# Kernel optimization log

Measured on AMD Instinct MI355X. Metric: run time of the kernel, lower is better.

## Reference

```python
import jax, jax.numpy as jnp
import numpy as np

N, DIM, HEADS, DH, WS = 32768, 1024, 8, 64, 256
INNER = HEADS * DH
MASK_VAL = -1e10  # ATTN_MASK_VALUE
EPS = 1e-5


def setup_inputs() -> dict:
    key = jax.random.key(0)
    k0, k1, k2 = jax.random.split(key, 3)
    x = jax.random.normal(k0, (N, DIM), jnp.float32)
    # rotary sin/cos with interleaved-pair layout matching rotate_every_two
    inv_freq = 1.0 / (10000.0 ** (jnp.arange(0, DH, 2, dtype=jnp.float32) / DH))
    freqs = jnp.arange(N, dtype=jnp.float32)[:, None] * inv_freq[None, :]  # [N, DH/2]
    sin = jnp.repeat(jnp.sin(freqs), 2, axis=-1)  # [N, DH]
    cos = jnp.repeat(jnp.cos(freqs), 2, axis=-1)  # [N, DH]
    gamma = jnp.ones((DIM,), jnp.float32)
    beta = jnp.zeros((DIM,), jnp.float32)
    w_qkv = jax.random.normal(k1, (DIM, 3 * INNER), jnp.float32) * 0.02
    w_out = jax.random.normal(k2, (INNER, DIM), jnp.float32) * 0.02
    b_out = jnp.zeros((DIM,), jnp.float32)
    return dict(x=x, sin=sin, cos=cos, gamma=gamma, beta=beta,
                w_qkv=w_qkv, w_out=w_out, b_out=b_out)


def _rotate_every_two(t):
    t1, t2 = t[..., 0::2], t[..., 1::2]
    return jnp.stack((-t2, t1), axis=-1).reshape(t.shape)


def _apply_rotary(t, sin, cos):
    # rot_dim == DH (full rotary), so no pass-through slice needed
    return t * cos + _rotate_every_two(t) * sin


def reference(x, sin, cos, gamma, beta, w_qkv, w_out, b_out):
    # LayerNorm (elementwise affine)
    mu = jnp.mean(x, axis=-1, keepdims=True)
    var = jnp.var(x, axis=-1, keepdims=True)
    x = (x - mu) * jax.lax.rsqrt(var + EPS) * gamma + beta
    # token shift: shift first half of channels by one token
    half = DIM // 2
    x_shift = jnp.pad(x[:, :half], ((1, 0), (0, 0)))[:-1]
    x = jnp.concatenate([x_shift, x[:, half:]], axis=-1)
    # qkv projection (no bias)
    qkv = x @ w_qkv  # [N, 3*INNER]
    q, k, v = jnp.split(qkv, 3, axis=-1)
    to_heads = lambda t: t.reshape(N, HEADS, DH).transpose(1, 0, 2)  # [H, N, DH]
    q, k, v = to_heads(q), to_heads(k), to_heads(v)
    # inline rotary on q, k AND v (as in source)
    q = _apply_rotary(q, sin, cos)
    k = _apply_rotary(k, sin, cos)
    v = _apply_rotary(v, sin, cos)
    # window split: [H, w, WS, DH]
    w = N // WS
    q, k, v = (t.reshape(HEADS, w, WS, DH) for t in (q, k, v))
    # look-back: each window attends to (previous window ++ current window)
    def lookback(t):
        t = jnp.pad(t, ((0, 0), (1, 0), (0, 0), (0, 0)))  # zero window at front
        return jnp.concatenate([t[:, :-1], t[:, 1:]], axis=2)  # [H, w, 2*WS, DH]
    k, v = lookback(k), lookback(v)
    sim = jnp.einsum('hwid,hwjd->hwij', q, k) * (DH ** -0.5)  # [H, w, WS, 2*WS]
    mask = jnp.tril(jnp.ones((WS, 2 * WS), dtype=bool), k=WS)  # j <= i + WS (causal)
    sim = jnp.where(mask, sim, MASK_VAL)
    attn = jax.nn.softmax(sim, axis=-1)
    out = jnp.einsum('hwij,hwjd->hwid', attn, v)  # [H, w, WS, DH]
    out = out.transpose(1, 2, 0, 3).reshape(N, INNER)  # '(w n) (h d)'
    return out @ w_out + b_out
```

## Files before the change

### kernel.cpp

```cpp
#include <hip/hip_runtime.h>

typedef __attribute__((ext_vector_type(4))) unsigned short us4;
typedef __attribute__((ext_vector_type(8))) unsigned short us8;
typedef __attribute__((ext_vector_type(8))) short s8;
typedef __attribute__((ext_vector_type(4))) float f32x4;
typedef __attribute__((ext_vector_type(16))) float f32x16;

#define NTOK 32768
#define DIM_ 1024
#define HEADS_ 8
#define DH_ 64
#define WS_ 256
#define NWIN_ 128
#define INNER_ 512

__device__ __forceinline__ float b2f(unsigned short u) {
  union { unsigned u; float f; } x; x.u = ((unsigned)u) << 16; return x.f;
}
__device__ __forceinline__ unsigned short f2b(float f) {
  union { float f; unsigned u; } x; x.f = f;
  unsigned r = x.u + 0x7FFFu + ((x.u >> 16) & 1u);
  return (unsigned short)(r >> 16);
}
__device__ __forceinline__ unsigned pk2(float a, float b) {
  return (unsigned)f2b(a) | ((unsigned)f2b(b) << 16);
}
__device__ __forceinline__ s8 mk_s8(unsigned w0, unsigned w1, unsigned w2, unsigned w3) {
  union { unsigned u[4]; s8 v; } x;
  x.u[0] = w0; x.u[1] = w1; x.u[2] = w2; x.u[3] = w3;
  return x.v;
}

__device__ __forceinline__ void gload_lds16(const unsigned short* g, void* l) {
  __builtin_amdgcn_global_load_lds((const __attribute__((address_space(1))) void*)g,
                                   (__attribute__((address_space(3))) void*)l, 16, 0, 0);
}

__global__ __launch_bounds__(256) void ln_shift(const float* __restrict__ x,
                                                const float* __restrict__ gamma,
                                                const float* __restrict__ beta,
                                                unsigned short* __restrict__ xs) {
  int row = blockIdx.x;
  int t = threadIdx.x;
  f32x4 v = ((const f32x4*)(x + (size_t)row * DIM_))[t];
  float sum = 0.f, ss = 0.f;
#pragma unroll
  for (int j = 0; j < 4; j++) { sum += v[j]; ss += v[j] * v[j]; }
#pragma unroll
  for (int off = 32; off >= 1; off >>= 1) {
    sum += __shfl_xor(sum, off);
    ss  += __shfl_xor(ss, off);
  }
  __shared__ float red[2][4];
  int wave = t >> 6, l = t & 63;
  if (l == 0) { red[0][wave] = sum; red[1][wave] = ss; }
  __syncthreads();
  sum = red[0][0] + red[0][1] + red[0][2] + red[0][3];
  ss  = red[1][0] + red[1][1] + red[1][2] + red[1][3];
  float mu = sum * (1.0f / DIM_);
  float var = ss * (1.0f / DIM_) - mu * mu;
  float rs = rsqrtf(var + 1e-5f);
  f32x4 g = ((const f32x4*)gamma)[t];
  f32x4 bb = ((const f32x4*)beta)[t];
  us4 o;
#pragma unroll
  for (int j = 0; j < 4; j++) o[j] = f2b((v[j] - mu) * rs * g[j] + bb[j]);
  int c0 = t * 4;
  if (c0 >= 512) {
    *(us4*)(xs + (size_t)row * DIM_ + c0) = o;
  } else {
    if (row + 1 < NTOK) *(us4*)(xs + (size_t)(row + 1) * DIM_ + c0) = o;
    if (row == 0) { us4 z = {0, 0, 0, 0}; *(us4*)(xs + c0) = z; }
  }
}

__global__ __launch_bounds__(256) void transpose_f32_bf16(const float* __restrict__ in,
                                                          unsigned short* __restrict__ out,
                                                          int R, int C) {
  __shared__ unsigned short tile[32][33];
  int bx = blockIdx.x * 32, by = blockIdx.y * 32;
  int tx = threadIdx.x, ty = threadIdx.y;
#pragma unroll
  for (int i = 0; i < 32; i += 8) tile[ty + i][tx] = f2b(in[(size_t)(by + ty + i) * C + bx + tx]);
  __syncthreads();
#pragma unroll
  for (int i = 0; i < 32; i += 8) out[(size_t)(bx + ty + i) * R + by + tx] = tile[tx][ty + i];
}

template <bool F32OUT>
__global__ __launch_bounds__(512, 2) void gemm_nt_pipe(const unsigned short* __restrict__ A,
                                                       const unsigned short* __restrict__ Bt,
                                                       void* __restrict__ Cv,
                                                       const float* __restrict__ bias,
                                                       int M, int N, int K) {
  __shared__ __align__(16) char lds[131072];
  int t = threadIdx.x;
  int l = t & 63, lg = l >> 4, ll = l & 15;
  int wave = t >> 6;
  int wm = wave >> 2, wn = wave & 3;

  int nbx = gridDim.x;
  int nwg = nbx * gridDim.y;
  int flat = blockIdx.y * nbx + blockIdx.x;
  int swz = (flat & 7) * (nwg >> 3) + (flat >> 3);
  int m0 = (swz / nbx) * 256, n0 = (swz % nbx) * 256;

  const f32x4 fz = {0.f, 0.f, 0.f, 0.f};
  f32x4 acc[8][4];
#pragma unroll
  for (int m = 0; m < 8; m++)
#pragma unroll
    for (int n = 0; n < 4; n++) acc[m][n] = fz;

  int srow = t >> 2;
  int sunit = (t & 3) ^ ((t >> 3) & 3);
  const unsigned short* gA = A + (size_t)(m0 + srow) * K + sunit * 8;
  const unsigned short* gB = Bt + (size_t)(n0 + srow) * K + sunit * 8;
  char* myA = lds + wave * 1024;
  char* myB = lds + 16384 + wave * 1024;

  int fsw = (ll >> 1) & 3;
  int nk = K >> 5;

#pragma unroll
  for (int s = 0; s < 3; s++) {
    gload_lds16(gA + s * 32, myA + s * 32768);
    gload_lds16(gA + s * 32 + (size_t)128 * K, myA + s * 32768 + 8192);
    gload_lds16(gB + s * 32, myB + s * 32768);
    gload_lds16(gB + s * 32 + (size_t)128 * K, myB + s * 32768 + 8192);
  }

  for (int kt = 0; kt < nk - 3; ++kt) {
    const char* sa = lds + (kt & 3) * 32768;
    const char* sb = sa + 16384;
    int pslot = ((kt + 3) & 3) * 32768;
    gload_lds16(gA + (kt + 3) * 32, myA + pslot);
    gload_lds16(gA + (kt + 3) * 32 + (size_t)128 * K, myA + pslot + 8192);
    asm volatile("s_waitcnt vmcnt(10)" ::: "memory");
    __builtin_amdgcn_s_barrier();
    __builtin_amdgcn_sched_barrier(0);
    s8 af[4], bf[4];
#pragma unroll
    for (int n = 0; n < 4; n++) {
      int r = wn * 64 + n * 16 + ll;
      bf[n] = *(const s8*)(sb + r * 64 + ((lg ^ fsw) << 4));
    }
#pragma unroll
    for (int m = 0; m < 4; m++) {
      int r = wm * 128 + m * 16 + ll;
      af[m] = *(const s8*)(sa + r * 64 + ((lg ^ fsw) << 4));
    }
    __builtin_amdgcn_s_setprio(1);
#pragma unroll
    for (int m = 0; m < 4; m++)
#pragma unroll
      for (int n = 0; n < 4; n++)
        acc[m][n] = __builtin_amdgcn_mfma_f32_16x16x32_bf16(af[m], bf[n], acc[m][n], 0, 0, 0);
    __builtin_amdgcn_s_setprio(0);
    gload_lds16(gB + (kt + 3) * 32, myB + pslot);
    gload_lds16(gB + (kt + 3) * 32 + (size_t)128 * K, myB + pslot + 8192);
    s8 af2[4];
#pragma unroll
    for (int m = 0; m < 4; m++) {
      int r = wm * 128 + 64 + m * 16 + ll;
      af2[m] = *(const s8*)(sa + r * 64 + ((lg ^ fsw) << 4));
    }
    __builtin_amdgcn_s_setprio(1);
#pragma unroll
    for (int m = 0; m < 4; m++)
#pragma unroll
      for (int n = 0; n < 4; n++)
        acc[m + 4][n] = __builtin_amdgcn_mfma_f32_16x16x32_bf16(af2[m], bf[n], acc[m + 4][n], 0, 0, 0);
    __builtin_amdgcn_s_setprio(0);
    __builtin_amdgcn_sched_barrier(0);
    __builtin_amdgcn_s_barrier();
  }

  asm volatile("s_waitcnt vmcnt(0)" ::: "memory");
  __builtin_amdgcn_s_barrier();
  __builtin_amdgcn_sched_barrier(0);
  for (int kt = nk - 3; kt < nk; ++kt) {
    const char* sa = lds + (kt & 3) * 32768;
    const char* sb = sa + 16384;
    s8 af[4], bf[4], af2[4];
#pragma unroll
    for (int n = 0; n < 4; n++) {
      int r = wn * 64 + n * 16 + ll;
      bf[n] = *(const s8*)(sb + r * 64 + ((lg ^ fsw) << 4));
    }
#pragma unroll
    for (int m = 0; m < 4; m++) {
      int r = wm * 128 + m * 16 + ll;
      af[m] = *(const s8*)(sa + r * 64 + ((lg ^ fsw) << 4));
    }
#pragma unroll
    for (int m = 0; m < 4; m++) {
      int r = wm * 128 + 64 + m * 16 + ll;
      af2[m] = *(const s8*)(sa + r * 64 + ((lg ^ fsw) << 4));
    }
#pragma unroll
    for (int m = 0; m < 4; m++)
#pragma unroll
      for (int n = 0; n < 4; n++)
        acc[m][n] = __builtin_amdgcn_mfma_f32_16x16x32_bf16(af[m], bf[n], acc[m][n], 0, 0, 0);
#pragma unroll
    for (int m = 0; m < 4; m++)
#pragma unroll
      for (int n = 0; n < 4; n++)
        acc[m + 4][n] = __builtin_amdgcn_mfma_f32_16x16x32_bf16(af2[m], bf[n], acc[m + 4][n], 0, 0, 0);
  }

#pragma unroll
  for (int n = 0; n < 4; n++) {
    int col = n0 + wn * 64 + n * 16 + ll;
    float bs = bias ? bias[col] : 0.0f;
#pragma unroll
    for (int m = 0; m < 8; m++) {
#pragma unroll
      for (int r = 0; r < 4; r++) {
        int row = m0 + wm * 128 + m * 16 + lg * 4 + r;
        if (F32OUT) ((float*)Cv)[(size_t)row * N + col] = acc[m][n][r] + bs;
        else ((unsigned short*)Cv)[(size_t)row * N + col] = f2b(acc[m][n][r] + bs);
      }
    }
  }
}

__global__ __launch_bounds__(256) void rotary_qk(const unsigned short* __restrict__ qkv,
                                                 const float* __restrict__ sn,
                                                 const float* __restrict__ cs,
                                                 unsigned short* __restrict__ qh,
                                                 unsigned short* __restrict__ kh) {
  int gid = blockIdx.x * 256 + threadIdx.x;
  int n = gid >> 7;
  int col = (gid & 127) * 8;
  int d = col & 63;
  us8 v = *(const us8*)(qkv + (size_t)n * 1536 + col);
  float se[8], ce[8];
  *(f32x4*)se = *(const f32x4*)(sn + (size_t)n * 64 + d);
  *(f32x4*)(se + 4) = *(const f32x4*)(sn + (size_t)n * 64 + d + 4);
  *(f32x4*)ce = *(const f32x4*)(cs + (size_t)n * 64 + d);
  *(f32x4*)(ce + 4) = *(const f32x4*)(cs + (size_t)n * 64 + d + 4);
  us8 o;
#pragma unroll
  for (int p = 0; p < 4; p++) {
    float v0 = b2f(v[2 * p]), v1 = b2f(v[2 * p + 1]);
    o[2 * p]     = f2b(v0 * ce[2 * p] - v1 * se[2 * p]);
    o[2 * p + 1] = f2b(v1 * ce[2 * p + 1] + v0 * se[2 * p + 1]);
  }
  int third = col >> 9;
  int cw = col & 511;
  int h = cw >> 6;
  unsigned short* dst = third ? kh : qh;
  *(us8*)(dst + ((size_t)h * NTOK + n) * 64 + (cw & 63)) = o;
}

__global__ __launch_bounds__(256) void rotary_vT(const unsigned short* __restrict__ qkv,
                                                 const float* __restrict__ sn,
                                                 const float* __restrict__ cs,
                                                 unsigned short* __restrict__ vt) {
  __shared__ unsigned short tile[64][72];
  int nt = blockIdx.x, h = blockIdx.y;
  int t = threadIdx.x;
  int i = t >> 2;
  int cc = (t & 3) * 16;
  int n = nt * 64 + i;
  const unsigned short* src = qkv + (size_t)n * 1536 + 1024 + h * 64 + cc;
  us8 v0 = *(const us8*)src;
  us8 v1 = *(const us8*)(src + 8);
  float se[16], ce[16];
#pragma unroll
  for (int q = 0; q < 4; q++) {
    *(f32x4*)(se + 4 * q) = *(const f32x4*)(sn + (size_t)n * 64 + cc + 4 * q);
    *(f32x4*)(ce + 4 * q) = *(const f32x4*)(cs + (size_t)n * 64 + cc + 4 * q);
  }
#pragma unroll
  for (int p = 0; p < 4; p++) {
    float a0 = b2f(v0[2 * p]), a1 = b2f(v0[2 * p + 1]);
    tile[i][cc + 2 * p]     = f2b(a0 * ce[2 * p] - a1 * se[2 * p]);
    tile[i][cc + 2 * p + 1] = f2b(a1 * ce[2 * p + 1] + a0 * se[2 * p + 1]);
    float b0 = b2f(v1[2 * p]), b1 = b2f(v1[2 * p + 1]);
    tile[i][cc + 8 + 2 * p]     = f2b(b0 * ce[8 + 2 * p] - b1 * se[8 + 2 * p]);
    tile[i][cc + 8 + 2 * p + 1] = f2b(b1 * ce[8 + 2 * p + 1] + b0 * se[8 + 2 * p + 1]);
  }
  __syncthreads();
  int dd = t >> 2;
  int nc = (t & 3) * 16;
  us8 r0, r1;
#pragma unroll
  for (int j = 0; j < 8; j++) { r0[j] = tile[nc + j][dd]; r1[j] = tile[nc + 8 + j][dd]; }
  unsigned short* dst = vt + ((size_t)h * 64 + dd) * NTOK + (size_t)nt * 64 + nc;
  *(us8*)dst = r0;
  *(us8*)(dst + 8) = r1;
}

__global__ __launch_bounds__(256, 4) void attn_kernel(const unsigned short* __restrict__ qh,
                                                      const unsigned short* __restrict__ kh,
                                                      const unsigned short* __restrict__ vt,
                                                      unsigned short* __restrict__ ao) {
  __shared__ char kbuf[2][8192];
  __shared__ char vbuf[8192];
  int half = blockIdx.x, w = blockIdx.y, h = blockIdx.z;
  int t = threadIdx.x;
  int wave = t >> 6, l = t & 63;
  int l31 = l & 31, hi = l >> 5;
  const unsigned short* qb = qh + (size_t)h * NTOK * 64;
  const unsigned short* kb = kh + (size_t)h * NTOK * 64;
  const unsigned short* vb = vt + (size_t)h * 64 * NTOK;

  int qw = half * 128 + wave * 32 + l31;
  int qn = w * 256 + qw;
  s8 qf[4];
#pragma unroll
  for (int dht = 0; dht < 4; dht++)
    qf[dht] = *(const s8*)(qb + (size_t)qn * 64 + dht * 16 + hi * 8);

  f32x16 o0 = {}, o1 = {};
  float dsum = (w == 0) ? 128.f : 0.f;
  int n0 = w * 256 - 256;
  int c0 = (w == 0) ? 4 : 0;

  int srow = wave * 16 + (l >> 3);
  int sunit = l & 7;

  {
    const unsigned short* g = kb + (size_t)(n0 + c0 * 64 + srow) * 64 + ((sunit ^ (srow & 7)) * 8);
    gload_lds16(g, kbuf[c0 & 1] + wave * 2048);
    gload_lds16(g + 8 * 64, kbuf[c0 & 1] + wave * 2048 + 1024);
  }
  __syncthreads();

  for (int c = c0; c < 8; ++c) {
    int cb = n0 + c * 64;
    {
      int d = srow;
      const unsigned short* g = vb + (size_t)d * NTOK + cb + ((sunit ^ (d & 7)) * 8);
      gload_lds16(g, vbuf + wave * 2048);
      gload_lds16(g + (size_t)8 * NTOK, vbuf + wave * 2048 + 1024);
    }
    if (c < 7) {
      const unsigned short* g = kb + (size_t)(cb + 64 + srow) * 64 + ((sunit ^ (srow & 7)) * 8);
      gload_lds16(g, kbuf[(c + 1) & 1] + wave * 2048);
      gload_lds16(g + 8 * 64, kbuf[(c + 1) & 1] + wave * 2048 + 1024);
    }

    f32x16 s[2] = {{}, {}};
    const char* kl = kbuf[c & 1];
#pragma unroll
    for (int kt = 0; kt < 2; kt++) {
#pragma unroll
      for (int dht = 0; dht < 4; dht++) {
        int row = kt * 32 + l31;
        int unit = (dht * 2 + hi) ^ (row & 7);
        s8 kf = *(const s8*)(kl + row * 128 + unit * 16);
        s[kt] = __builtin_amdgcn_mfma_f32_32x32x16_bf16(kf, qf[dht], s[kt], 0, 0, 0);
      }
    }

    unsigned P0[2][4], P1[2][4];
#pragma unroll
    for (int kt = 0; kt < 2; kt++) {
#pragma unroll
      for (int r = 0; r < 16; r++) {
        int j = c * 64 + kt * 32 + (r & 3) + 8 * (r >> 2) + hi * 4;
        float e = (j <= qw + 256) ? __expf(s[kt][r] * 0.125f) : 0.f;
        s[kt][r] = e;
        dsum += e;
      }
#pragma unroll
      for (int j2 = 0; j2 < 4; j2++) {
        P0[kt][j2] = pk2(s[kt][j2 * 4 + 0], s[kt][j2 * 4 + 1]);
        P1[kt][j2] = pk2(s[kt][j2 * 4 + 2], s[kt][j2 * 4 + 3]);
      }
    }

    __syncthreads();

#pragma unroll
    for (int tt = 0; tt < 4; tt++) {
      int kt = tt >> 1, ss = tt & 1;
      unsigned a = P0[kt][2 * ss], b = P1[kt][2 * ss];
      unsigned cx = P0[kt][2 * ss + 1], dx = P1[kt][2 * ss + 1];
      asm volatile("v_permlane32_swap_b32 %0, %1" : "+v"(a), "+v"(cx));
      asm volatile("v_permlane32_swap_b32 %0, %1" : "+v"(b), "+v"(dx));
      s8 pf = mk_s8(a, b, cx, dx);
      {
        int row = l31;
        int unit = (tt * 2 + hi) ^ (row & 7);
        s8 vf = *(const s8*)(vbuf + row * 128 + unit * 16);
        o0 = __builtin_amdgcn_mfma_f32_32x32x16_bf16(vf, pf, o0, 0, 0, 0);
      }
      {
        int row = 32 + l31;
        int unit = (tt * 2 + hi) ^ (row & 7);
        s8 vf = *(const s8*)(vbuf + row * 128 + unit * 16);
        o1 = __builtin_amdgcn_mfma_f32_32x32x16_bf16(vf, pf, o1, 0, 0, 0);
      }
    }
    __syncthreads();
  }

  dsum += __shfl_xor(dsum, 32);
  float inv = 1.f / dsum;

  unsigned short* orow = ao + (size_t)qn * INNER_ + h * 64;
#pragma unroll
  for (int g = 0; g < 4; g++) {
    us4 st0, st1;
#pragma unroll
    for (int rr = 0; rr < 4; rr++) {
      st0[rr] = f2b(o0[g * 4 + rr] * inv);
      st1[rr] = f2b(o1[g * 4 + rr] * inv);
    }
    *(us4*)(orow + g * 8 + hi * 4) = st0;
    *(us4*)(orow + 32 + g * 8 + hi * 4) = st1;
  }
}

extern "C" void kernel_launch(void* const* d_in, const int* in_sizes, int n_in,
                              void* d_out, int out_size, void* d_ws, size_t ws_size,
                              hipStream_t stream) {
  const float* x     = (const float*)d_in[0];
  const float* sin_  = (const float*)d_in[1];
  const float* cos_  = (const float*)d_in[2];
  const float* gamma = (const float*)d_in[3];
  const float* beta  = (const float*)d_in[4];
  const float* w_qkv = (const float*)d_in[5];
  const float* w_out = (const float*)d_in[6];
  const float* b_out = (const float*)d_in[7];

  char* ws = (char*)d_ws;
  const size_t OFF_WQT = 0;
  const size_t OFF_WOT = 3145728;
  const size_t OFF_XS  = 4194304;
  const size_t OFF_QKV = 71303168;
  const size_t OFF_VT  = 171966464;
  const size_t NEEDED  = 205520896;
  if (ws_size < NEEDED) return;

  unsigned short* wqT = (unsigned short*)(ws + OFF_WQT);
  unsigned short* woT = (unsigned short*)(ws + OFF_WOT);
  unsigned short* xs  = (unsigned short*)(ws + OFF_XS);
  unsigned short* qkv = (unsigned short*)(ws + OFF_QKV);
  unsigned short* vt  = (unsigned short*)(ws + OFF_VT);
  unsigned short* qh  = xs;
  unsigned short* kh  = (unsigned short*)(ws + OFF_XS + 33554432);
  unsigned short* ao  = qkv;

  transpose_f32_bf16<<<dim3(1536 / 32, 1024 / 32), dim3(32, 8), 0, stream>>>(w_qkv, wqT, 1024, 1536);
  transpose_f32_bf16<<<dim3(1024 / 32, 512 / 32), dim3(32, 8), 0, stream>>>(w_out, woT, 512, 1024);
  ln_shift<<<NTOK, 256, 0, stream>>>(x, gamma, beta, xs);
  gemm_nt_pipe<false><<<dim3(1536 / 256, NTOK / 256), 512, 0, stream>>>(xs, wqT, qkv, nullptr, NTOK, 1536, 1024);
  rotary_qk<<<(NTOK * 128) / 256, 256, 0, stream>>>(qkv, sin_, cos_, qh, kh);
  rotary_vT<<<dim3(NTOK / 64, HEADS_), 256, 0, stream>>>(qkv, sin_, cos_, vt);
  attn_kernel<<<dim3(2, NWIN_, HEADS_), 256, 0, stream>>>(qh, kh, vt, ao);
  gemm_nt_pipe<true><<<dim3(1024 / 256, NTOK / 256), 512, 0, stream>>>(ao, woT, (void*)d_out, b_out, NTOK, 1024, 512);
}
```

Before: 354.3 us.

## Restructure GEMM to double-buffered BK=64 pipeline with spread global prefetches

Changes the GEMM main loop from a 4-stage ring of K=32 tiles to two LDS buffers of K=64 tiles, with a new 8-way XOR swizzle on 128-byte rows. Global-to-LDS prefetches for the next tile are spread across the four MFMA phases so memory traffic overlaps with compute. The aim is to halve the number of barriers per K step and cut loop overhead. The cost is a shallower prefetch depth (one tile ahead), which may expose more memory latency.

```diff
diff --git a/kernel.cpp b/kernel.cpp
--- a/kernel.cpp
+++ b/kernel.cpp
@@ -88,11 +88,11 @@
 }
 
 template <bool F32OUT>
-__global__ __launch_bounds__(512, 2) void gemm_nt_pipe(const unsigned short* __restrict__ A,
-                                                       const unsigned short* __restrict__ Bt,
-                                                       void* __restrict__ Cv,
-                                                       const float* __restrict__ bias,
-                                                       int M, int N, int K) {
+__global__ __launch_bounds__(512, 2) void gemm_nt_p8(const unsigned short* __restrict__ A,
+                                                     const unsigned short* __restrict__ Bt,
+                                                     void* __restrict__ Cv,
+                                                     const float* __restrict__ bias,
+                                                     int M, int N, int K) {
   __shared__ __align__(16) char lds[131072];
   int t = threadIdx.x;
   int l = t & 63, lg = l >> 4, ll = l & 15;
@@ -112,102 +112,106 @@
 #pragma unroll
     for (int n = 0; n < 4; n++) acc[m][n] = fz;
 
-  int srow = t >> 2;
-  int sunit = (t & 3) ^ ((t >> 3) & 3);
+  int srow = t >> 3;
+  int sunit = (t & 7) ^ (srow & 7);
   const unsigned short* gA = A + (size_t)(m0 + srow) * K + sunit * 8;
   const unsigned short* gB = Bt + (size_t)(n0 + srow) * K + sunit * 8;
-  char* myA = lds + wave * 1024;
-  char* myB = lds + 16384 + wave * 1024;
-
-  int fsw = (ll >> 1) & 3;
-  int nk = K >> 5;
-
-#pragma unroll
-  for (int s = 0; s < 3; s++) {
-    gload_lds16(gA + s * 32, myA + s * 32768);
-    gload_lds16(gA + s * 32 + (size_t)128 * K, myA + s * 32768 + 8192);
-    gload_lds16(gB + s * 32, myB + s * 32768);
-    gload_lds16(gB + s * 32 + (size_t)128 * K, myB + s * 32768 + 8192);
-  }
-
-  for (int kt = 0; kt < nk - 3; ++kt) {
-    const char* sa = lds + (kt & 3) * 32768;
-    const char* sb = sa + 16384;
-    int pslot = ((kt + 3) & 3) * 32768;
-    gload_lds16(gA + (kt + 3) * 32, myA + pslot);
-    gload_lds16(gA + (kt + 3) * 32 + (size_t)128 * K, myA + pslot + 8192);
-    asm volatile("s_waitcnt vmcnt(10)" ::: "memory");
+  int t16 = t * 16;
+  int nk = K >> 6;
+
+#pragma unroll
+  for (int j = 0; j < 4; j++) {
+    gload_lds16(gA + (size_t)(j * 64) * K, lds + j * 8192 + t16);
+    gload_lds16(gB + (size_t)(j * 64) * K, lds + 32768 + j * 8192 + t16);
+  }
+
+  for (int kt = 0; kt < nk - 1; ++kt) {
+    const char* sa = lds + (kt & 1) * 65536;
+    const char* sb = sa + 32768;
+    char* dA = lds + ((kt + 1) & 1) * 65536;
+    char* dB = dA + 32768;
+    const unsigned short* nA = gA + (kt + 1) * 64;
+    const unsigned short* nB = gB + (kt + 1) * 64;
+
+    gload_lds16(nA, dA + t16);
+    gload_lds16(nA + (size_t)64 * K, dA + 8192 + t16);
+    asm volatile("s_waitcnt vmcnt(2)" ::: "memory");
+    __builtin_amdgcn_sched_barrier(0);
     __builtin_amdgcn_s_barrier();
     __builtin_amdgcn_sched_barrier(0);
-    s8 af[4], bf[4];
-#pragma unroll
-    for (int n = 0; n < 4; n++) {
-      int r = wn * 64 + n * 16 + ll;
-      bf[n] = *(const s8*)(sb + r * 64 + ((lg ^ fsw) << 4));
-    }
-#pragma unroll
-    for (int m = 0; m < 4; m++) {
-      int r = wm * 128 + m * 16 + ll;
-      af[m] = *(const s8*)(sa + r * 64 + ((lg ^ fsw) << 4));
-    }
-    __builtin_amdgcn_s_setprio(1);
-#pragma unroll
-    for (int m = 0; m < 4; m++)
-#pragma unroll
-      for (int n = 0; n < 4; n++)
-        acc[m][n] = __builtin_amdgcn_mfma_f32_16x16x32_bf16(af[m], bf[n], acc[m][n], 0, 0, 0);
-    __builtin_amdgcn_s_setprio(0);
-    gload_lds16(gB + (kt + 3) * 32, myB + pslot);
-    gload_lds16(gB + (kt + 3) * 32 + (size_t)128 * K, myB + pslot + 8192);
-    s8 af2[4];
-#pragma unroll
-    for (int m = 0; m < 4; m++) {
-      int r = wm * 128 + 64 + m * 16 + ll;
-      af2[m] = *(const s8*)(sa + r * 64 + ((lg ^ fsw) << 4));
-    }
-    __builtin_amdgcn_s_setprio(1);
-#pragma unroll
-    for (int m = 0; m < 4; m++)
-#pragma unroll
-      for (int n = 0; n < 4; n++)
-        acc[m + 4][n] = __builtin_amdgcn_mfma_f32_16x16x32_bf16(af2[m], bf[n], acc[m + 4][n], 0, 0, 0);
-    __builtin_amdgcn_s_setprio(0);
+
+    s8 bf[4];
+#pragma unroll
+    for (int p = 0; p < 4; ++p) {
+      const int qm = p & 1, kk = p >> 1;
+      s8 af[4];
+#pragma unroll
+      for (int m = 0; m < 4; m++) {
+        int r = wm * 128 + qm * 64 + m * 16 + ll;
+        af[m] = *(const s8*)(sa + r * 128 + (((kk * 4 + lg) ^ (r & 7)) << 4));
+      }
+      if (qm == 0) {
+#pragma unroll
+        for (int n = 0; n < 4; n++) {
+          int r = wn * 64 + n * 16 + ll;
+          bf[n] = *(const s8*)(sb + r * 128 + (((kk * 4 + lg) ^ (r & 7)) << 4));
+        }
+      }
+      if (p == 0) {
+        gload_lds16(nA + (size_t)128 * K, dA + 16384 + t16);
+        gload_lds16(nA + (size_t)192 * K, dA + 24576 + t16);
+      } else if (p == 1) {
+        gload_lds16(nB, dB + t16);
+        gload_lds16(nB + (size_t)64 * K, dB + 8192 + t16);
+      } else if (p == 2) {
+        gload_lds16(nB + (size_t)128 * K, dB + 16384 + t16);
+        gload_lds16(nB + (size_t)192 * K, dB + 24576 + t16);
+      }
+      __builtin_amdgcn_s_setprio(1);
+#pragma unroll
+      for (int m = 0; m < 4; m++)
+#pragma unroll
+        for (int n = 0; n < 4; n++)
+          acc[qm * 4 + m][n] =
+              __builtin_amdgcn_mfma_f32_16x16x32_bf16(af[m], bf[n], acc[qm * 4 + m][n], 0, 0, 0);
+      __builtin_amdgcn_s_setprio(0);
+    }
     __builtin_amdgcn_sched_barrier(0);
     __builtin_amdgcn_s_barrier();
   }
 
-  asm volatile("s_waitcnt vmcnt(0)" ::: "memory");
-  __builtin_amdgcn_s_barrier();
-  __builtin_amdgcn_sched_barrier(0);
-  for (int kt = nk - 3; kt < nk; ++kt) {
-    const char* sa = lds + (kt & 3) * 32768;
-    const char* sb = sa + 16384;
-    s8 af[4], bf[4], af2[4];
-#pragma unroll
-    for (int n = 0; n < 4; n++) {
-      int r = wn * 64 + n * 16 + ll;
-      bf[n] = *(const s8*)(sb + r * 64 + ((lg ^ fsw) << 4));
-    }
-#pragma unroll
-    for (int m = 0; m < 4; m++) {
-      int r = wm * 128 + m * 16 + ll;
-      af[m] = *(const s8*)(sa + r * 64 + ((lg ^ fsw) << 4));
-    }
-#pragma unroll
-    for (int m = 0; m < 4; m++) {
-      int r = wm * 128 + 64 + m * 16 + ll;
-      af2[m] = *(const s8*)(sa + r * 64 + ((lg ^ fsw) << 4));
-    }
-#pragma unroll
-    for (int m = 0; m < 4; m++)
-#pragma unroll
-      for (int n = 0; n < 4; n++)
-        acc[m][n] = __builtin_amdgcn_mfma_f32_16x16x32_bf16(af[m], bf[n], acc[m][n], 0, 0, 0);
-#pragma unroll
-    for (int m = 0; m < 4; m++)
-#pragma unroll
-      for (int n = 0; n < 4; n++)
-        acc[m + 4][n] = __builtin_amdgcn_mfma_f32_16x16x32_bf16(af2[m], bf[n], acc[m + 4][n], 0, 0, 0);
+  {
+    int kt = nk - 1;
+    const char* sa = lds + (kt & 1) * 65536;
+    const char* sb = sa + 32768;
+    asm volatile("s_waitcnt vmcnt(0)" ::: "memory");
+    __builtin_amdgcn_sched_barrier(0);
+    __builtin_amdgcn_s_barrier();
+    __builtin_amdgcn_sched_barrier(0);
+    s8 bf[4];
+#pragma unroll
+    for (int p = 0; p < 4; ++p) {
+      const int qm = p & 1, kk = p >> 1;
+      s8 af[4];
+#pragma unroll
+      for (int m = 0; m < 4; m++) {
+        int r = wm * 128 + qm * 64 + m * 16 + ll;
+        af[m] = *(const s8*)(sa + r * 128 + (((kk * 4 + lg) ^ (r & 7)) << 4));
+      }
+      if (qm == 0) {
+#pragma unroll
+        for (int n = 0; n < 4; n++) {
+          int r = wn * 64 + n * 16 + ll;
+          bf[n] = *(const s8*)(sb + r * 128 + (((kk * 4 + lg) ^ (r & 7)) << 4));
+        }
+      }
+#pragma unroll
+      for (int m = 0; m < 4; m++)
+#pragma unroll
+        for (int n = 0; n < 4; n++)
+          acc[qm * 4 + m][n] =
+              __builtin_amdgcn_mfma_f32_16x16x32_bf16(af[m], bf[n], acc[qm * 4 + m][n], 0, 0, 0);
+    }
   }
 
 #pragma unroll
@@ -450,9 +454,9 @@
   transpose_f32_bf16<<<dim3(1536 / 32, 1024 / 32), dim3(32, 8), 0, stream>>>(w_qkv, wqT, 1024, 1536);
   transpose_f32_bf16<<<dim3(1024 / 32, 512 / 32), dim3(32, 8), 0, stream>>>(w_out, woT, 512, 1024);
   ln_shift<<<NTOK, 256, 0, stream>>>(x, gamma, beta, xs);
-  gemm_nt_pipe<false><<<dim3(1536 / 256, NTOK / 256), 512, 0, stream>>>(xs, wqT, qkv, nullptr, NTOK, 1536, 1024);
+  gemm_nt_p8<false><<<dim3(1536 / 256, NTOK / 256), 512, 0, stream>>>(xs, wqT, qkv, nullptr, NTOK, 1536, 1024);
   rotary_qk<<<(NTOK * 128) / 256, 256, 0, stream>>>(qkv, sin_, cos_, qh, kh);
   rotary_vT<<<dim3(NTOK / 64, HEADS_), 256, 0, stream>>>(qkv, sin_, cos_, vt);
   attn_kernel<<<dim3(2, NWIN_, HEADS_), 256, 0, stream>>>(qh, kh, vt, ao);
-  gemm_nt_pipe<true><<<dim3(1024 / 256, NTOK / 256), 512, 0, stream>>>(ao, woT, (void*)d_out, b_out, NTOK, 1024, 512);
-}
+  gemm_nt_p8<true><<<dim3(1024 / 256, NTOK / 256), 512, 0, stream>>>(ao, woT, (void*)d_out, b_out, NTOK, 1024, 512);
+}
```

Result: faster. 342.9 us (-3.2%).

## Fuse rotary into QKV GEMM epilogue and shrink GEMM pipeline to double buffer

Applied to the files above, without the earlier changes.

Applies rotary embedding to q, k and v inside the QKV GEMM epilogue, using lane shuffles to regroup accumulator pairs, and writes head-major q/k plus a rotated v buffer directly. This removes the separate rotary kernels and the round trip of the qkv intermediate through memory, leaving a plain transpose for V. The GEMM pipeline also drops from four-stage to two-stage LDS buffering (64KB), with launch bounds raised to allow more blocks per CU. The trade-off is less prefetch depth, more register pressure in the epilogue, and an extra vh buffer for V.

```diff
diff --git a/kernel.cpp b/kernel.cpp
--- a/kernel.cpp
+++ b/kernel.cpp
@@ -87,13 +87,18 @@
   for (int i = 0; i < 32; i += 8) out[(size_t)(bx + ty + i) * R + by + tx] = tile[tx][ty + i];
 }
 
-template <bool F32OUT>
-__global__ __launch_bounds__(512, 2) void gemm_nt_pipe(const unsigned short* __restrict__ A,
-                                                       const unsigned short* __restrict__ Bt,
-                                                       void* __restrict__ Cv,
-                                                       const float* __restrict__ bias,
-                                                       int M, int N, int K) {
-  __shared__ __align__(16) char lds[131072];
+template <bool F32OUT, bool ROPE>
+__global__ __launch_bounds__(512, 4) void gemm_nt_p9(const unsigned short* __restrict__ A,
+                                                     const unsigned short* __restrict__ Bt,
+                                                     void* __restrict__ Cv,
+                                                     const float* __restrict__ bias,
+                                                     const float* __restrict__ sinp,
+                                                     const float* __restrict__ cosp,
+                                                     unsigned short* __restrict__ qh,
+                                                     unsigned short* __restrict__ kh,
+                                                     unsigned short* __restrict__ vh,
+                                                     int M, int N, int K) {
+  __shared__ __align__(16) char lds[65536];
   int t = threadIdx.x;
   int l = t & 63, lg = l >> 4, ll = l & 15;
   int wave = t >> 6;
@@ -116,29 +121,30 @@
   int sunit = (t & 3) ^ ((t >> 3) & 3);
   const unsigned short* gA = A + (size_t)(m0 + srow) * K + sunit * 8;
   const unsigned short* gB = Bt + (size_t)(n0 + srow) * K + sunit * 8;
-  char* myA = lds + wave * 1024;
-  char* myB = lds + 16384 + wave * 1024;
-
+  int t16 = t * 16;
   int fsw = (ll >> 1) & 3;
   int nk = K >> 5;
 
-#pragma unroll
-  for (int s = 0; s < 3; s++) {
-    gload_lds16(gA + s * 32, myA + s * 32768);
-    gload_lds16(gA + s * 32 + (size_t)128 * K, myA + s * 32768 + 8192);
-    gload_lds16(gB + s * 32, myB + s * 32768);
-    gload_lds16(gB + s * 32 + (size_t)128 * K, myB + s * 32768 + 8192);
-  }
-
-  for (int kt = 0; kt < nk - 3; ++kt) {
-    const char* sa = lds + (kt & 3) * 32768;
+  gload_lds16(gA, lds + t16);
+  gload_lds16(gA + (size_t)128 * K, lds + 8192 + t16);
+  gload_lds16(gB, lds + 16384 + t16);
+  gload_lds16(gB + (size_t)128 * K, lds + 24576 + t16);
+
+  for (int kt = 0; kt < nk - 1; ++kt) {
+    const char* sa = lds + (kt & 1) * 32768;
     const char* sb = sa + 16384;
-    int pslot = ((kt + 3) & 3) * 32768;
-    gload_lds16(gA + (kt + 3) * 32, myA + pslot);
-    gload_lds16(gA + (kt + 3) * 32 + (size_t)128 * K, myA + pslot + 8192);
-    asm volatile("s_waitcnt vmcnt(10)" ::: "memory");
+    char* dA = lds + ((kt + 1) & 1) * 32768;
+    char* dB = dA + 16384;
+    const unsigned short* nA = gA + (kt + 1) * 32;
+    const unsigned short* nB = gB + (kt + 1) * 32;
+
+    gload_lds16(nA, dA + t16);
+    gload_lds16(nA + (size_t)128 * K, dA + 8192 + t16);
+    asm volatile("s_waitcnt vmcnt(2)" ::: "memory");
+    __builtin_amdgcn_sched_barrier(0);
     __builtin_amdgcn_s_barrier();
     __builtin_amdgcn_sched_barrier(0);
+
     s8 af[4], bf[4];
 #pragma unroll
     for (int n = 0; n < 4; n++) {
@@ -150,6 +156,8 @@
       int r = wm * 128 + m * 16 + ll;
       af[m] = *(const s8*)(sa + r * 64 + ((lg ^ fsw) << 4));
     }
+    gload_lds16(nB, dB + t16);
+    gload_lds16(nB + (size_t)128 * K, dB + 8192 + t16);
     __builtin_amdgcn_s_setprio(1);
 #pragma unroll
     for (int m = 0; m < 4; m++)
@@ -157,8 +165,6 @@
       for (int n = 0; n < 4; n++)
         acc[m][n] = __builtin_amdgcn_mfma_f32_16x16x32_bf16(af[m], bf[n], acc[m][n], 0, 0, 0);
     __builtin_amdgcn_s_setprio(0);
-    gload_lds16(gB + (kt + 3) * 32, myB + pslot);
-    gload_lds16(gB + (kt + 3) * 32 + (size_t)128 * K, myB + pslot + 8192);
     s8 af2[4];
 #pragma unroll
     for (int m = 0; m < 4; m++) {
@@ -176,12 +182,14 @@
     __builtin_amdgcn_s_barrier();
   }
 
-  asm volatile("s_waitcnt vmcnt(0)" ::: "memory");
-  __builtin_amdgcn_s_barrier();
-  __builtin_amdgcn_sched_barrier(0);
-  for (int kt = nk - 3; kt < nk; ++kt) {
-    const char* sa = lds + (kt & 3) * 32768;
+  {
+    int kt = nk - 1;
+    const char* sa = lds + (kt & 1) * 32768;
     const char* sb = sa + 16384;
+    asm volatile("s_waitcnt vmcnt(0)" ::: "memory");
+    __builtin_amdgcn_sched_barrier(0);
+    __builtin_amdgcn_s_barrier();
+    __builtin_amdgcn_sched_barrier(0);
     s8 af[4], bf[4], af2[4];
 #pragma unroll
     for (int n = 0; n < 4; n++) {
@@ -210,79 +218,78 @@
         acc[m + 4][n] = __builtin_amdgcn_mfma_f32_16x16x32_bf16(af2[m], bf[n], acc[m + 4][n], 0, 0, 0);
   }
 
-#pragma unroll
-  for (int n = 0; n < 4; n++) {
-    int col = n0 + wn * 64 + n * 16 + ll;
-    float bs = bias ? bias[col] : 0.0f;
+  if (ROPE) {
+    int b = ll & 3, q = ll >> 2;
+    int third = n0 >> 9;
+    bool bo1 = (b & 1) != 0, bo2 = (b & 2) != 0;
 #pragma unroll
     for (int m = 0; m < 8; m++) {
-#pragma unroll
-      for (int r = 0; r < 4; r++) {
-        int row = m0 + wm * 128 + m * 16 + lg * 4 + r;
-        if (F32OUT) ((float*)Cv)[(size_t)row * N + col] = acc[m][n][r] + bs;
-        else ((unsigned short*)Cv)[(size_t)row * N + col] = f2b(acc[m][n][r] + bs);
-      }
-    }
-  }
-}
-
-__global__ __launch_bounds__(256) void rotary_qk(const unsigned short* __restrict__ qkv,
-                                                 const float* __restrict__ sn,
-                                                 const float* __restrict__ cs,
-                                                 unsigned short* __restrict__ qh,
-                                                 unsigned short* __restrict__ kh) {
-  int gid = blockIdx.x * 256 + threadIdx.x;
-  int n = gid >> 7;
-  int col = (gid & 127) * 8;
-  int d = col & 63;
-  us8 v = *(const us8*)(qkv + (size_t)n * 1536 + col);
-  float se[8], ce[8];
-  *(f32x4*)se = *(const f32x4*)(sn + (size_t)n * 64 + d);
-  *(f32x4*)(se + 4) = *(const f32x4*)(sn + (size_t)n * 64 + d + 4);
-  *(f32x4*)ce = *(const f32x4*)(cs + (size_t)n * 64 + d);
-  *(f32x4*)(ce + 4) = *(const f32x4*)(cs + (size_t)n * 64 + d + 4);
-  us8 o;
-#pragma unroll
-  for (int p = 0; p < 4; p++) {
-    float v0 = b2f(v[2 * p]), v1 = b2f(v[2 * p + 1]);
-    o[2 * p]     = f2b(v0 * ce[2 * p] - v1 * se[2 * p]);
-    o[2 * p + 1] = f2b(v1 * ce[2 * p + 1] + v0 * se[2 * p + 1]);
-  }
-  int third = col >> 9;
-  int cw = col & 511;
-  int h = cw >> 6;
-  unsigned short* dst = third ? kh : qh;
-  *(us8*)(dst + ((size_t)h * NTOK + n) * 64 + (cw & 63)) = o;
-}
-
-__global__ __launch_bounds__(256) void rotary_vT(const unsigned short* __restrict__ qkv,
-                                                 const float* __restrict__ sn,
-                                                 const float* __restrict__ cs,
-                                                 unsigned short* __restrict__ vt) {
-  __shared__ unsigned short tile[64][72];
+      int row = m0 + wm * 128 + ((m >> 2) ? 64 : 0) + (m & 3) * 16 + lg * 4 + b;
+#pragma unroll
+      for (int n = 0; n < 4; n++) {
+        float v0 = acc[m][n][0], v1 = acc[m][n][1], v2 = acc[m][n][2], v3 = acc[m][n][3];
+        float x0 = __shfl_xor(v1, 1);
+        float x1 = __shfl_xor(v0, 1);
+        float x2 = __shfl_xor(v3, 1);
+        float x3 = __shfl_xor(v2, 1);
+        float u0 = bo1 ? x0 : v0;
+        float u1 = bo1 ? v1 : x1;
+        float u2 = bo1 ? x2 : v2;
+        float u3 = bo1 ? v3 : x3;
+        float y0 = __shfl_xor(u2, 2);
+        float y1 = __shfl_xor(u3, 2);
+        float y2 = __shfl_xor(u0, 2);
+        float y3 = __shfl_xor(u1, 2);
+        float w0 = bo2 ? y0 : u0;
+        float w1 = bo2 ? y1 : u1;
+        float w2 = bo2 ? u2 : y2;
+        float w3 = bo2 ? u3 : y3;
+        int cb = n0 + wn * 64 + n * 16 + q * 4;
+        int cit = cb & 511;
+        int head = cit >> 6, d0 = cit & 63;
+        f32x4 s4 = *(const f32x4*)(sinp + (size_t)row * 64 + d0);
+        f32x4 c4 = *(const f32x4*)(cosp + (size_t)row * 64 + d0);
+        us4 st;
+        st[0] = f2b(w0 * c4[0] - w1 * s4[0]);
+        st[1] = f2b(w1 * c4[1] + w0 * s4[1]);
+        st[2] = f2b(w2 * c4[2] - w3 * s4[2]);
+        st[3] = f2b(w3 * c4[3] + w2 * s4[3]);
+        if (third == 0)      *(us4*)(qh + ((size_t)head * NTOK + row) * 64 + d0) = st;
+        else if (third == 1) *(us4*)(kh + ((size_t)head * NTOK + row) * 64 + d0) = st;
+        else                 *(us4*)(vh + (size_t)row * 512 + cit) = st;
+      }
+    }
+  } else {
+#pragma unroll
+    for (int n = 0; n < 4; n++) {
+      int col = n0 + wn * 64 + n * 16 + ll;
+      float bs = bias ? bias[col] : 0.0f;
+#pragma unroll
+      for (int m = 0; m < 8; m++) {
+#pragma unroll
+        for (int r = 0; r < 4; r++) {
+          int row = m0 + wm * 128 + ((m >> 2) ? 64 : 0) + (m & 3) * 16 + lg * 4 + r;
+          if (F32OUT) ((float*)Cv)[(size_t)row * N + col] = acc[m][n][r] + bs;
+          else ((unsigned short*)Cv)[(size_t)row * N + col] = f2b(acc[m][n][r] + bs);
+        }
+      }
+    }
+  }
+}
+
+__global__ __launch_bounds__(256) void transpose_v(const unsigned short* __restrict__ vh,
+                                                   unsigned short* __restrict__ vt) {
+  __shared__ unsigned short tile[64][80];
   int nt = blockIdx.x, h = blockIdx.y;
   int t = threadIdx.x;
   int i = t >> 2;
   int cc = (t & 3) * 16;
   int n = nt * 64 + i;
-  const unsigned short* src = qkv + (size_t)n * 1536 + 1024 + h * 64 + cc;
+  const unsigned short* src = vh + (size_t)n * 512 + h * 64 + cc;
   us8 v0 = *(const us8*)src;
   us8 v1 = *(const us8*)(src + 8);
-  float se[16], ce[16];
-#pragma unroll
-  for (int q = 0; q < 4; q++) {
-    *(f32x4*)(se + 4 * q) = *(const f32x4*)(sn + (size_t)n * 64 + cc + 4 * q);
-    *(f32x4*)(ce + 4 * q) = *(const f32x4*)(cs + (size_t)n * 64 + cc + 4 * q);
-  }
-#pragma unroll
-  for (int p = 0; p < 4; p++) {
-    float a0 = b2f(v0[2 * p]), a1 = b2f(v0[2 * p + 1]);
-    tile[i][cc + 2 * p]     = f2b(a0 * ce[2 * p] - a1 * se[2 * p]);
-    tile[i][cc + 2 * p + 1] = f2b(a1 * ce[2 * p + 1] + a0 * se[2 * p + 1]);
-    float b0 = b2f(v1[2 * p]), b1 = b2f(v1[2 * p + 1]);
-    tile[i][cc + 8 + 2 * p]     = f2b(b0 * ce[8 + 2 * p] - b1 * se[8 + 2 * p]);
-    tile[i][cc + 8 + 2 * p + 1] = f2b(b1 * ce[8 + 2 * p + 1] + b0 * se[8 + 2 * p + 1]);
-  }
+  *(us8*)&tile[i][cc] = v0;
+  *(us8*)&tile[i][cc + 8] = v1;
   __syncthreads();
   int dd = t >> 2;
   int nc = (t & 3) * 16;
@@ -433,7 +440,9 @@
   const size_t OFF_WQT = 0;
   const size_t OFF_WOT = 3145728;
   const size_t OFF_XS  = 4194304;
-  const size_t OFF_QKV = 71303168;
+  const size_t OFF_QH  = 71303168;
+  const size_t OFF_KH  = 104857600;
+  const size_t OFF_VH  = 138412032;
   const size_t OFF_VT  = 171966464;
   const size_t NEEDED  = 205520896;
   if (ws_size < NEEDED) return;
@@ -441,18 +450,19 @@
   unsigned short* wqT = (unsigned short*)(ws + OFF_WQT);
   unsigned short* woT = (unsigned short*)(ws + OFF_WOT);
   unsigned short* xs  = (unsigned short*)(ws + OFF_XS);
-  unsigned short* qkv = (unsigned short*)(ws + OFF_QKV);
+  unsigned short* qh  = (unsigned short*)(ws + OFF_QH);
+  unsigned short* kh  = (unsigned short*)(ws + OFF_KH);
+  unsigned short* vh  = (unsigned short*)(ws + OFF_VH);
   unsigned short* vt  = (unsigned short*)(ws + OFF_VT);
-  unsigned short* qh  = xs;
-  unsigned short* kh  = (unsigned short*)(ws + OFF_XS + 33554432);
-  unsigned short* ao  = qkv;
+  unsigned short* ao  = xs;
 
   transpose_f32_bf16<<<dim3(1536 / 32, 1024 / 32), dim3(32, 8), 0, stream>>>(w_qkv, wqT, 1024, 1536);
   transpose_f32_bf16<<<dim3(1024 / 32, 512 / 32), dim3(32, 8), 0, stream>>>(w_out, woT, 512, 1024);
   ln_shift<<<NTOK, 256, 0, stream>>>(x, gamma, beta, xs);
-  gemm_nt_pipe<false><<<dim3(1536 / 256, NTOK / 256), 512, 0, stream>>>(xs, wqT, qkv, nullptr, NTOK, 1536, 1024);
-  rotary_qk<<<(NTOK * 128) / 256, 256, 0, stream>>>(qkv, sin_, cos_, qh, kh);
-  rotary_vT<<<dim3(NTOK / 64, HEADS_), 256, 0, stream>>>(qkv, sin_, cos_, vt);
+  gemm_nt_p9<false, true><<<dim3(1536 / 256, NTOK / 256), 512, 0, stream>>>(
+      xs, wqT, nullptr, nullptr, sin_, cos_, qh, kh, vh, NTOK, 1536, 1024);
+  transpose_v<<<dim3(NTOK / 64, HEADS_), 256, 0, stream>>>(vh, vt);
   attn_kernel<<<dim3(2, NWIN_, HEADS_), 256, 0, stream>>>(qh, kh, vt, ao);
-  gemm_nt_pipe<true><<<dim3(1024 / 256, NTOK / 256), 512, 0, stream>>>(ao, woT, (void*)d_out, b_out, NTOK, 1024, 512);
-}
+  gemm_nt_p9<true, false><<<dim3(1024 / 256, NTOK / 256), 512, 0, stream>>>(
+      ao, woT, (void*)d_out, b_out, nullptr, nullptr, nullptr, nullptr, nullptr, NTOK, 1024, 512);
+}
```

Result: slower. 1.375 ms (+288.1%).
